# Kernel tuning notes

Hardware: AMD Instinct MI355X
Metric: run time of the kernel (lower is better)

Reference implementation:

```python
import jax, jax.numpy as jnp
import numpy as np

EPS_NORM = 1e-12
EPS_POS = 1e-05
MARGIN = 0.5


def l2_norm(x):
    # matches torch: x / sqrt(sum(x^2, axis=1) + 1e-12)
    norm = jnp.sqrt(jnp.sum(x * x, axis=1) + EPS_NORM)
    return x / norm[:, None]


def setup_inputs() -> dict:
    key = jax.random.key(0)
    k1, k2, k3, k4 = jax.random.split(key, 4)
    n, d, n_classes = 8192, 1024, 1024
    inputs_col = jax.random.normal(k1, (n, d), dtype=jnp.float32)
    inputs_row = jax.random.normal(k2, (n, d), dtype=jnp.float32)
    targets_col = jax.random.randint(k3, (n,), 0, n_classes)
    target_row = jax.random.randint(k4, (n,), 0, n_classes)
    return {"inputs_col": inputs_col, "targets_col": targets_col,
            "inputs_row": inputs_row, "target_row": target_row}


def reference(inputs_col, targets_col, inputs_row, target_row):
    n = inputs_col.shape[0]
    # [n, n] cosine similarity matrix
    sim = l2_norm(inputs_col) @ l2_norm(inputs_row).T
    same = targets_col[:, None] == target_row[None, :]  # [n, n] bool
    pos_mask = same & (sim < 1.0 - EPS_POS)
    neg_mask = (~same) & (sim > MARGIN)
    pos_loss = jnp.sum(jnp.where(pos_mask, 1.0 - sim, 0.0), axis=1)  # [n]
    neg_loss = jnp.sum(jnp.where(neg_mask, sim, 0.0), axis=1)        # [n]
    has_pos = jnp.any(pos_mask, axis=1)  # rows without valid positives are skipped
    row_loss = jnp.where(has_pos, pos_loss + neg_loss, 0.0)
    return jnp.sum(row_loss) / n
```

## Files before the change

### kernel.cpp

```cpp
#include <hip/hip_runtime.h>


constexpr int N = 8192;
constexpr int D = 1024;
constexpr int NT = D / 64;

typedef short bf16x8 __attribute__((ext_vector_type(8)));
typedef float f32x4 __attribute__((ext_vector_type(4)));

static __device__ inline unsigned short f2bf(float f) {
  unsigned int u = __float_as_uint(f);
  unsigned int r = (u + 0x7fffu + ((u >> 16) & 1u)) >> 16;
  return (unsigned short)r;
}

__global__ __launch_bounds__(256) void normalize_kernel(
    const float* __restrict__ in_col, const float* __restrict__ in_row,
    unsigned short* __restrict__ out_col, unsigned short* __restrict__ out_row) {
  int row = blockIdx.x;
  const float* in;
  unsigned short* out;
  if (row < N) {
    in = in_col + (size_t)row * D;
    out = out_col + (size_t)row * D;
  } else {
    in = in_row + (size_t)(row - N) * D;
    out = out_row + (size_t)(row - N) * D;
  }
  int tid = threadIdx.x;
  float4 v = ((const float4*)in)[tid];
  float s = v.x * v.x + v.y * v.y + v.z * v.z + v.w * v.w;
#pragma unroll
  for (int off = 32; off >= 1; off >>= 1) s += __shfl_xor(s, off, 64);
  __shared__ float wsum[4];
  int lane = tid & 63, wid = tid >> 6;
  if (lane == 0) wsum[wid] = s;
  __syncthreads();
  float tot = wsum[0] + wsum[1] + wsum[2] + wsum[3];
  float inv = 1.0f / sqrtf(tot + 1e-12f);
  ushort4 o;
  o.x = f2bf(v.x * inv);
  o.y = f2bf(v.y * inv);
  o.z = f2bf(v.z * inv);
  o.w = f2bf(v.w * inv);
  ((ushort4*)out)[tid] = o;
}

__global__ __launch_bounds__(512, 2) void loss_kernel(
    const unsigned short* __restrict__ An, const unsigned short* __restrict__ Bn,
    const int* __restrict__ tc, const int* __restrict__ tr,
    float* __restrict__ lossG, int* __restrict__ hasG) {
  __shared__ unsigned short lds[65536];

  const int tid = threadIdx.x;
  const int lane = tid & 63;
  const int wid = tid >> 6;
  const int wr = wid >> 2;
  const int wc = wid & 3;

  const int bid = blockIdx.x;
  const int swz = (bid & 7) * 128 + (bid >> 3);
  const int iBase = (swz >> 5) * 256;
  const int jBase = (swz & 31) * 256;

  const int frow = lane & 15;
  const int fkb = (lane >> 4) * 16;
  const int rxor = (lane & 7) << 4;
  const int kx0 = (0 + fkb) ^ rxor;
  const int kx1 = (64 + fkb) ^ rxor;
  int rowA[4], rowB[2];
#pragma unroll
  for (int m2 = 0; m2 < 4; m2++) rowA[m2] = (wr * 64 + m2 * 16 + frow) * 128;
#pragma unroll
  for (int n2 = 0; n2 < 2; n2++) rowB[n2] = (wc * 32 + n2 * 16 + frow) * 128;

  const int rl0 = tid >> 3;
  const int kel = (tid & 7) * 8;
  const int kSw = kel ^ ((rl0 & 7) << 3);
  const int rA0 = iBase + rl0;
  const int rB0 = jBase + ((rl0 >> 5) * 64) + (rl0 & 31);

#define GLDS(g, l)                                                        \
  __builtin_amdgcn_global_load_lds(                                       \
      (const __attribute__((address_space(1))) void*)(g),                 \
      (__attribute__((address_space(3))) void*)(l), 16, 0, 0)

#define STAGE_A(h, tt)                                                          \
  do {                                                                          \
    const int _k = ((tt) & 15) * 64 + kSw;                                      \
    unsigned short* _d = lds + ((((tt) & 1) * 2 + (h)) * 8192) + wid * 512;     \
    GLDS(An + (size_t)(rA0 + (h) * 64) * D + _k, _d);                           \
    GLDS(An + (size_t)(rA0 + 128 + (h) * 64) * D + _k, _d + 4096);              \
  } while (0)
#define STAGE_B(h, tt)                                                          \
  do {                                                                          \
    const int _k = ((tt) & 15) * 64 + kSw;                                      \
    unsigned short* _d = lds + 32768 + ((((tt) & 1) * 2 + (h)) * 8192) + wid * 512; \
    GLDS(Bn + (size_t)(rB0 + (h) * 32) * D + _k, _d);                           \
    GLDS(Bn + (size_t)(rB0 + 128 + (h) * 32) * D + _k, _d + 4096);              \
  } while (0)

  f32x4 acc[8][4];
#pragma unroll
  for (int mi = 0; mi < 8; mi++)
#pragma unroll
    for (int ni = 0; ni < 4; ni++) acc[mi][ni] = (f32x4){0.f, 0.f, 0.f, 0.f};

  bf16x8 af[4][2], bf[2][2];
  const char* ldsc = (const char*)lds;

  STAGE_A(0, 0);
  STAGE_B(0, 0);
  STAGE_B(1, 0);
  STAGE_A(1, 0);
  STAGE_A(0, 1);
  asm volatile("s_waitcnt vmcnt(6)" ::: "memory");
  __builtin_amdgcn_sched_barrier(0);
  __builtin_amdgcn_s_barrier();

#define PHASE(MIH, NIH, LOADA, STG)                                             \
  do {                                                                          \
    if (LOADA) {                                                                \
      _Pragma("unroll") for (int m2 = 0; m2 < 4; m2++) {                        \
        af[m2][0] = *(const bf16x8*)(ldsc + dA + (MIH) * 16384 + rowA[m2] + kx0); \
        af[m2][1] = *(const bf16x8*)(ldsc + dA + (MIH) * 16384 + rowA[m2] + kx1); \
      }                                                                         \
    }                                                                           \
    _Pragma("unroll") for (int n2 = 0; n2 < 2; n2++) {                          \
      bf[n2][0] = *(const bf16x8*)(ldsc + dB + (NIH) * 16384 + rowB[n2] + kx0);  \
      bf[n2][1] = *(const bf16x8*)(ldsc + dB + (NIH) * 16384 + rowB[n2] + kx1);  \
    }                                                                           \
    STG;                                                                        \
    __builtin_amdgcn_s_barrier();                                               \
    asm volatile("s_waitcnt lgkmcnt(0)");                                       \
    __builtin_amdgcn_sched_barrier(0);                                          \
    __builtin_amdgcn_s_setprio(1);                                              \
    _Pragma("unroll") for (int m2 = 0; m2 < 4; m2++)                            \
        _Pragma("unroll") for (int n2 = 0; n2 < 2; n2++)                        \
            _Pragma("unroll") for (int kk = 0; kk < 2; kk++)                    \
                acc[(MIH) * 4 + m2][(NIH) * 2 + n2] =                           \
                    __builtin_amdgcn_mfma_f32_16x16x32_bf16(                    \
                        af[m2][kk], bf[n2][kk],                                 \
                        acc[(MIH) * 4 + m2][(NIH) * 2 + n2], 0, 0, 0);          \
    __builtin_amdgcn_s_setprio(0);                                              \
    asm volatile("s_waitcnt vmcnt(6)" ::: "memory");                            \
    __builtin_amdgcn_sched_barrier(0);                                          \
    __builtin_amdgcn_s_barrier();                                               \
  } while (0)

  for (int t = 0; t < NT; ++t) {
    const int dA = (t & 1) * 32768;
    const int dB = 65536 + (t & 1) * 32768;
    PHASE(0, 0, true, STAGE_B(0, t + 1));
    PHASE(0, 1, false, STAGE_B(1, t + 1));
    PHASE(1, 0, true, STAGE_A(1, t + 1));
    PHASE(1, 1, false, STAGE_A(0, t + 2));
  }
#undef PHASE
#undef STAGE_A
#undef STAGE_B
#undef GLDS

  int trj[4];
#pragma unroll
  for (int ni = 0; ni < 4; ni++) trj[ni] = tr[jBase + wc * 64 + ni * 16 + frow];

#pragma unroll
  for (int mi = 0; mi < 8; mi++) {
#pragma unroll
    for (int r = 0; r < 4; r++) {
      const int i = iBase + wr * 128 + mi * 16 + (lane >> 4) * 4 + r;
      const int tci = tc[i];
      float v = 0.f;
      bool hasp = false;
#pragma unroll
      for (int ni = 0; ni < 4; ni++) {
        float s = acc[mi][ni][r];
        if (tci == trj[ni]) {
          if (s < 1.0f - 1e-5f) { v += 1.0f - s; hasp = true; }
        } else if (s > 0.5f) {
          v += s;
        }
      }
#pragma unroll
      for (int off = 1; off < 16; off <<= 1) v += __shfl_xor(v, off, 16);
      unsigned long long m = __ballot(hasp);
      bool rowHas = ((m >> ((lane >> 4) * 16)) & 0xFFFFull) != 0;
      if ((lane & 15) == 0) {
        if (v != 0.f) atomicAdd(&lossG[i], v);
        if (rowHas) atomicOr(&hasG[i], 1);
      }
    }
  }
}

__global__ __launch_bounds__(256) void finalize_kernel(
    const float* __restrict__ lossG, const int* __restrict__ hasG,
    float* __restrict__ out) {
  int tid = threadIdx.x;
  float s = 0.f;
  for (int i = tid; i < N; i += 256)
    if (hasG[i]) s += lossG[i];
#pragma unroll
  for (int off = 32; off >= 1; off >>= 1) s += __shfl_xor(s, off, 64);
  __shared__ float w4[4];
  if ((tid & 63) == 0) w4[tid >> 6] = s;
  __syncthreads();
  if (tid == 0) out[0] = (w4[0] + w4[1] + w4[2] + w4[3]) / (float)N;
}

extern "C" void kernel_launch(void* const* d_in, const int* in_sizes, int n_in,
                              void* d_out, int out_size, void* d_ws, size_t ws_size,
                              hipStream_t stream) {
  const float* in_col = (const float*)d_in[0];
  const int* tcol = (const int*)d_in[1];
  const float* in_row = (const float*)d_in[2];
  const int* trow = (const int*)d_in[3];
  float* out = (float*)d_out;

  char* ws = (char*)d_ws;
  float* lossG = (float*)ws;
  int* hasG = (int*)(ws + (size_t)N * 4);
  unsigned short* colN = (unsigned short*)(ws + (size_t)N * 8);
  unsigned short* rowN = colN + (size_t)N * D;

  hipMemsetAsync(ws, 0, (size_t)N * 8, stream);
  normalize_kernel<<<2 * N, 256, 0, stream>>>(in_col, in_row, colN, rowN);
  loss_kernel<<<1024, 512, 0, stream>>>(colN, rowN, tcol, trow, lossG, hasG);
  finalize_kernel<<<1, 256, 0, stream>>>(lossG, hasG, out);
}
```

Before: 309.6 us.

## Reorder GEMM phase schedule, reuse fragments, and retile block-to-tile mapping

```diff
diff --git a/kernel.cpp b/kernel.cpp
--- a/kernel.cpp
+++ b/kernel.cpp
@@ -59,9 +59,9 @@
   const int wc = wid & 3;
 
   const int bid = blockIdx.x;
-  const int swz = (bid & 7) * 128 + (bid >> 3);
-  const int iBase = (swz >> 5) * 256;
-  const int jBase = (swz & 31) * 256;
+  const int x = bid & 7, s = bid >> 3;
+  const int iBase = (((s & 7) | ((s >> 5) << 3))) * 256;
+  const int jBase = (x * 4 + ((s >> 3) & 3)) * 256;
 
   const int frow = lane & 15;
   const int fkb = (lane >> 4) * 16;
@@ -85,19 +85,19 @@
       (const __attribute__((address_space(1))) void*)(g),                 \
       (__attribute__((address_space(3))) void*)(l), 16, 0, 0)
 
-#define STAGE_A(h, tt)                                                          \
-  do {                                                                          \
-    const int _k = ((tt) & 15) * 64 + kSw;                                      \
-    unsigned short* _d = lds + ((((tt) & 1) * 2 + (h)) * 8192) + wid * 512;     \
-    GLDS(An + (size_t)(rA0 + (h) * 64) * D + _k, _d);                           \
-    GLDS(An + (size_t)(rA0 + 128 + (h) * 64) * D + _k, _d + 4096);              \
-  } while (0)
-#define STAGE_B(h, tt)                                                          \
-  do {                                                                          \
-    const int _k = ((tt) & 15) * 64 + kSw;                                      \
-    unsigned short* _d = lds + 32768 + ((((tt) & 1) * 2 + (h)) * 8192) + wid * 512; \
-    GLDS(Bn + (size_t)(rB0 + (h) * 32) * D + _k, _d);                           \
-    GLDS(Bn + (size_t)(rB0 + 128 + (h) * 32) * D + _k, _d + 4096);              \
+#define STAGE_A(h, tt, P)                                                     \
+  do {                                                                        \
+    const int _k = ((tt) & 15) * 64 + kSw;                                    \
+    unsigned short* _d = lds + (((P) * 2 + (h)) * 8192) + wid * 512;          \
+    GLDS(An + (size_t)(rA0 + (h) * 64) * D + _k, _d);                         \
+    GLDS(An + (size_t)(rA0 + 128 + (h) * 64) * D + _k, _d + 4096);            \
+  } while (0)
+#define STAGE_B(h, tt, P)                                                     \
+  do {                                                                        \
+    const int _k = ((tt) & 15) * 64 + kSw;                                    \
+    unsigned short* _d = lds + 32768 + (((P) * 2 + (h)) * 8192) + wid * 512;  \
+    GLDS(Bn + (size_t)(rB0 + (h) * 32) * D + _k, _d);                         \
+    GLDS(Bn + (size_t)(rB0 + 128 + (h) * 32) * D + _k, _d + 4096);            \
   } while (0)
 
   f32x4 acc[8][4];
@@ -109,31 +109,32 @@
   bf16x8 af[4][2], bf[2][2];
   const char* ldsc = (const char*)lds;
 
-  STAGE_A(0, 0);
-  STAGE_B(0, 0);
-  STAGE_B(1, 0);
-  STAGE_A(1, 0);
-  STAGE_A(0, 1);
-  asm volatile("s_waitcnt vmcnt(6)" ::: "memory");
-  __builtin_amdgcn_sched_barrier(0);
+  STAGE_A(0, 0, 0);
+  STAGE_B(0, 0, 0);
+  STAGE_B(1, 0, 0);
+  STAGE_A(1, 0, 0);
+  STAGE_A(1, 1, 1);
+  asm volatile("s_waitcnt vmcnt(2)" ::: "memory");
   __builtin_amdgcn_s_barrier();
 
-#define PHASE(MIH, NIH, LOADA, STG)                                             \
+#define PH(MIH, NIH, LOADA, LOADB, DA, DB, STG, DRN)                            \
   do {                                                                          \
     if (LOADA) {                                                                \
       _Pragma("unroll") for (int m2 = 0; m2 < 4; m2++) {                        \
-        af[m2][0] = *(const bf16x8*)(ldsc + dA + (MIH) * 16384 + rowA[m2] + kx0); \
-        af[m2][1] = *(const bf16x8*)(ldsc + dA + (MIH) * 16384 + rowA[m2] + kx1); \
+        af[m2][0] = *(const bf16x8*)(ldsc + (DA) + (MIH) * 16384 + rowA[m2] + kx0); \
+        af[m2][1] = *(const bf16x8*)(ldsc + (DA) + (MIH) * 16384 + rowA[m2] + kx1); \
       }                                                                         \
     }                                                                           \
-    _Pragma("unroll") for (int n2 = 0; n2 < 2; n2++) {                          \
-      bf[n2][0] = *(const bf16x8*)(ldsc + dB + (NIH) * 16384 + rowB[n2] + kx0);  \
-      bf[n2][1] = *(const bf16x8*)(ldsc + dB + (NIH) * 16384 + rowB[n2] + kx1);  \
+    if (LOADB) {                                                                \
+      _Pragma("unroll") for (int n2 = 0; n2 < 2; n2++) {                        \
+        bf[n2][0] = *(const bf16x8*)(ldsc + (DB) + (NIH) * 16384 + rowB[n2] + kx0); \
+        bf[n2][1] = *(const bf16x8*)(ldsc + (DB) + (NIH) * 16384 + rowB[n2] + kx1); \
+      }                                                                         \
     }                                                                           \
     STG;                                                                        \
+    asm volatile("" ::: "memory");                                              \
     __builtin_amdgcn_s_barrier();                                               \
-    asm volatile("s_waitcnt lgkmcnt(0)");                                       \
-    __builtin_amdgcn_sched_barrier(0);                                          \
+    asm volatile("s_waitcnt lgkmcnt(0)" ::: "memory");                          \
     __builtin_amdgcn_s_setprio(1);                                              \
     _Pragma("unroll") for (int m2 = 0; m2 < 4; m2++)                            \
         _Pragma("unroll") for (int n2 = 0; n2 < 2; n2++)                        \
@@ -143,20 +144,34 @@
                         af[m2][kk], bf[n2][kk],                                 \
                         acc[(MIH) * 4 + m2][(NIH) * 2 + n2], 0, 0, 0);          \
     __builtin_amdgcn_s_setprio(0);                                              \
-    asm volatile("s_waitcnt vmcnt(6)" ::: "memory");                            \
-    __builtin_amdgcn_sched_barrier(0);                                          \
+    DRN;                                                                        \
+    asm volatile("" ::: "memory");                                              \
     __builtin_amdgcn_s_barrier();                                               \
   } while (0)
 
-  for (int t = 0; t < NT; ++t) {
-    const int dA = (t & 1) * 32768;
-    const int dB = 65536 + (t & 1) * 32768;
-    PHASE(0, 0, true, STAGE_B(0, t + 1));
-    PHASE(0, 1, false, STAGE_B(1, t + 1));
-    PHASE(1, 0, true, STAGE_A(1, t + 1));
-    PHASE(1, 1, false, STAGE_A(0, t + 2));
+#define DRAIN asm volatile("s_waitcnt vmcnt(2)" ::: "memory")
+
+#define TILE(T, P)                                                              \
+  do {                                                                          \
+    PH(0, 0, true, true, (P)*32768, 65536 + (P)*32768,                          \
+       STAGE_A(0, (T) + 1, 1 - (P)), );                                         \
+    PH(0, 1, false, true, (P)*32768, 65536 + (P)*32768,                         \
+       STAGE_B(0, (T) + 1, 1 - (P)), );                                         \
+    PH(1, 1, true, false, (P)*32768, 65536 + (P)*32768,                         \
+       STAGE_B(1, (T) + 1, 1 - (P)), );                                         \
+    PH(1, 0, false, true, (P)*32768, 65536 + (P)*32768,                         \
+       STAGE_A(1, (T) + 2, (P)), DRAIN);                                        \
+  } while (0)
+
+  for (int tp = 0; tp < NT / 2; ++tp) {
+    const int t0 = 2 * tp;
+    TILE(t0, 0);
+    TILE(t0 + 1, 1);
   }
-#undef PHASE
+  asm volatile("s_waitcnt vmcnt(0)" ::: "memory");
+#undef TILE
+#undef PH
+#undef DRAIN
 #undef STAGE_A
 #undef STAGE_B
 #undef GLDS
@@ -175,11 +190,11 @@
       bool hasp = false;
 #pragma unroll
       for (int ni = 0; ni < 4; ni++) {
-        float s = acc[mi][ni][r];
+        float s2 = acc[mi][ni][r];
         if (tci == trj[ni]) {
-          if (s < 1.0f - 1e-5f) { v += 1.0f - s; hasp = true; }
-        } else if (s > 0.5f) {
-          v += s;
+          if (s2 < 1.0f - 1e-5f) { v += 1.0f - s2; hasp = true; }
+        } else if (s2 > 0.5f) {
+          v += s2;
         }
       }
 #pragma unroll
```

New measurement: 297.8 us. 1.04x faster.
